# Optimization experiments

Hardware: AMD Instinct MI355X
Metric: run time of the kernel (lower is better)

## Reference

```python
import jax, jax.numpy as jnp
import numpy as np

NUM_EMBEDDINGS = 1024
EMBEDDING_DIM = 512
COMMITMENT_COST = 0.25


def setup_inputs() -> dict:
    key = jax.random.key(0)
    k1, k2 = jax.random.split(key)
    z_e = jax.random.normal(k1, (32, EMBEDDING_DIM, 32, 32), dtype=jnp.float32)
    # nn.Embedding weight, initialized normal (EMA branch: decay > 0)
    embedding = jax.random.normal(k2, (NUM_EMBEDDINGS, EMBEDDING_DIM), dtype=jnp.float32)
    return {"z_e": z_e, "embedding": embedding}


def reference(z_e, embedding):
    # z_e: [B, D, H, W] -> [B, H, W, D]
    ze = jnp.transpose(z_e, (0, 2, 3, 1))
    B, H, W, D = ze.shape
    K = embedding.shape[0]
    flat = ze.reshape(-1, D)  # [N, D]

    distances = (
        jnp.sum(flat * flat, axis=1, keepdims=True)
        + jnp.sum(embedding * embedding, axis=1)
        - 2.0 * jnp.matmul(flat, embedding.T)
    )
    indices = jnp.argmin(distances, axis=1)  # [N]

    # one-hot encodings (returned, and used for perplexity) -- matmul with
    # codebook is equivalent to a gather, so use the gather for z_q
    encodings = jax.nn.one_hot(indices, K, dtype=flat.dtype)  # [N, K]
    z_q = embedding[indices].reshape(B, H, W, D)

    # EMA branch (decay > 0): loss is commitment loss only
    e_latent_loss = jnp.mean((jax.lax.stop_gradient(z_q) - ze) ** 2)
    loss = COMMITMENT_COST * e_latent_loss

    # straight-through estimator
    z_q_st = ze + jax.lax.stop_gradient(z_q - ze)

    avg_probs = jnp.mean(encodings, axis=0)  # [K]
    perplexity = jnp.exp(-jnp.sum(avg_probs * jnp.log(avg_probs + 1e-10)))

    z_q_out = jnp.transpose(z_q_st, (0, 3, 1, 2))  # back to [B, D, H, W]
    return z_q_out, loss, perplexity, encodings
```

## Files before the change

### kernel.cpp

```cpp
#include <hip/hip_runtime.h>
#include <stdint.h>

#define B_ 32
#define D_ 512
#define P_ 1024
#define N_ 32768
#define K_ 1024

#define GAP_THR 0.75f

typedef unsigned long long u64;
typedef __attribute__((ext_vector_type(8))) short short8;
typedef __attribute__((ext_vector_type(4))) float float4v;

__device__ __forceinline__ unsigned fkey(float f) {
    unsigned u = __float_as_uint(f);
    return (u & 0x80000000u) ? ~u : (u | 0x80000000u);
}
__device__ __forceinline__ float funkey(unsigned k) {
    unsigned u = (k & 0x80000000u) ? (k & 0x7fffffffu) : ~k;
    return __uint_as_float(u);
}
__device__ __forceinline__ unsigned short f2bf(float x) {
    unsigned u = __float_as_uint(x);
    unsigned r = (u + 0x7fffu + ((u >> 16) & 1u)) >> 16;
    return (unsigned short)r;
}
__device__ __forceinline__ float bf2f(unsigned short h) {
    return __uint_as_float(((unsigned)h) << 16);
}

#define GLOAD_LDS16(gsrc, ldst) \
    __builtin_amdgcn_global_load_lds((const __attribute__((address_space(1))) unsigned int*)(const void*)(gsrc), \
                                     (__attribute__((address_space(3))) unsigned int*)(void*)(ldst), 16, 0, 0)

__global__ __launch_bounds__(256) void k_prep(const float* __restrict__ z,
                                              unsigned short* __restrict__ Xhi,
                                              const float* __restrict__ emb,
                                              unsigned short* __restrict__ Ehi,
                                              float* __restrict__ ET,
                                              float* __restrict__ enorm,
                                              double* __restrict__ enormD,
                                              int* __restrict__ counts,
                                              int* __restrict__ flagCount) {
    __shared__ float Zl[128][67];
    int tid = threadIdx.x;

    if (blockIdx.x >= 256) {
        int base = (blockIdx.x - 256) * 8;
        if (tid < 8) counts[base + tid] = 0;
        if (blockIdx.x == 256 && tid == 0) *flagCount = 0;
        int wave = tid >> 6, lane = tid & 63;
        float* Es = &Zl[0][0];
        #pragma unroll
        for (int cc = 0; cc < 2; ++cc) {
            int ci = wave * 2 + cc;
            int c = base + ci;
            const float4* row = (const float4*)(emb + (size_t)c * D_);
            float4 a = row[lane * 2];
            float4 b2 = row[lane * 2 + 1];
            float xs[8] = {a.x, a.y, a.z, a.w, b2.x, b2.y, b2.z, b2.w};
            unsigned short h[8];
            double s = 0.0;
            #pragma unroll
            for (int j = 0; j < 8; ++j) {
                h[j] = f2bf(xs[j]);
                Es[ci * 513 + lane * 8 + j] = xs[j];
                double d = (double)xs[j];
                s += d * d;
            }
            uint4 w;
            w.x = (unsigned)h[0] | ((unsigned)h[1] << 16);
            w.y = (unsigned)h[2] | ((unsigned)h[3] << 16);
            w.z = (unsigned)h[4] | ((unsigned)h[5] << 16);
            w.w = (unsigned)h[6] | ((unsigned)h[7] << 16);
            *(uint4*)(Ehi + (size_t)c * D_ + lane * 8) = w;
            #pragma unroll
            for (int off = 32; off; off >>= 1) s += __shfl_down(s, off, 64);
            if (lane == 0) { enorm[c] = (float)s; enormD[c] = s; }
        }
        __syncthreads();
        #pragma unroll
        for (int g = 0; g < 2; ++g) {
            int d = g * 256 + tid;
            float v[8];
            #pragma unroll
            for (int cc = 0; cc < 8; ++cc) v[cc] = Es[cc * 513 + d];
            float4* dst = (float4*)(ET + (size_t)d * 1024 + base);
            dst[0] = make_float4(v[0], v[1], v[2], v[3]);
            dst[1] = make_float4(v[4], v[5], v[6], v[7]);
        }
        return;
    }

    int b = blockIdx.x >> 3, pt = blockIdx.x & 7;
    int p0 = pt * 128;
    int t0 = b * P_ + p0;
    const float* zb = z + ((size_t)b * D_) * P_ + p0;
    int c8 = tid & 7, pp = tid >> 3;

    for (int dc = 0; dc < 8; ++dc) {
        int d0 = dc * 64;
        __syncthreads();
        #pragma unroll
        for (int jj = 0; jj < 8; ++jj) {
            int flat = jj * 256 + tid;
            int d = flat >> 5, p4 = flat & 31;
            float4 v = *(const float4*)(zb + (size_t)(d0 + d) * P_ + p4 * 4);
            Zl[p4 * 4 + 0][d] = v.x;
            Zl[p4 * 4 + 1][d] = v.y;
            Zl[p4 * 4 + 2][d] = v.z;
            Zl[p4 * 4 + 3][d] = v.w;
        }
        __syncthreads();
        #pragma unroll
        for (int g = 0; g < 4; ++g) {
            int p = pp + g * 32;
            unsigned short hh[8];
            #pragma unroll
            for (int j = 0; j < 8; ++j) hh[j] = f2bf(Zl[p][c8 * 8 + j]);
            uint4 w;
            w.x = (unsigned)hh[0] | ((unsigned)hh[1] << 16);
            w.y = (unsigned)hh[2] | ((unsigned)hh[3] << 16);
            w.z = (unsigned)hh[4] | ((unsigned)hh[5] << 16);
            w.w = (unsigned)hh[6] | ((unsigned)hh[7] << 16);
            *(uint4*)(Xhi + (size_t)(t0 + p) * D_ + d0 + c8 * 8) = w;
        }
    }
}

__global__ __launch_bounds__(512, 2) void k_gemm(const unsigned short* __restrict__ Xhi,
                                                 const unsigned short* __restrict__ Ehi,
                                                 const float* __restrict__ enorm,
                                                 u64* __restrict__ part) {
    __shared__ __align__(16) char smem[131072];
    const int tid = threadIdx.x;
    const int wave = tid >> 6, lane = tid & 63;
    const int lr = lane & 15, lg = lane >> 4;
    const int wr = wave >> 2, wc = wave & 3;
    const int work = (blockIdx.x & 7) * 64 + (blockIdx.x >> 3);
    const int rb = work >> 2, cb = work & 3;
    const int t0 = rb * 256, c0 = cb * 256;

    float4v acc[8][4];
    #pragma unroll
    for (int i = 0; i < 8; ++i)
        #pragma unroll
        for (int j = 0; j < 4; ++j)
            acc[i][j] = (float4v){0.f, 0.f, 0.f, 0.f};

    auto stageHalf = [&](int h) {
        if (h >= 32) return;
        int T = h >> 2, j = h & 3;
        int khalf = j >> 1, isB = j & 1;
        const unsigned short* plane = isB ? Xhi : Ehi;
        int row0 = isB ? t0 : c0;
        int kseg = T * 64 + khalf * 32;
        char* region = smem + (T & 1) * 65536 + isB * 32768 + khalf * 16384;
        #pragma unroll
        for (int jj = 0; jj < 2; ++jj) {
            int o = jj * 8192 + wave * 1024 + lane * 16;
            int pair = o >> 7;
            int sl = ((o >> 4) & 7) ^ (pair & 7);
            int row = pair * 2 + (sl >> 2);
            int k8 = sl & 3;
            GLOAD_LDS16(plane + (size_t)(row0 + row) * D_ + kseg + k8 * 8,
                        region + jj * 8192 + wave * 1024);
        }
    };

    for (int h = 0; h < 6; ++h) stageHalf(h);

    for (int t = 0; t < 8; ++t) {
        const int buf = t & 1;
        const char* Ab = smem + buf * 65536;
        const char* Bb = smem + buf * 65536 + 32768;
        if (t < 7) { asm volatile("s_waitcnt vmcnt(4)" ::: "memory"); }
        else       { asm volatile("s_waitcnt vmcnt(0)" ::: "memory"); }
        __builtin_amdgcn_s_barrier();
        __builtin_amdgcn_sched_barrier(0);
        #pragma unroll
        for (int q = 0; q < 4; ++q) {
            const int ks = q >> 1, mq = q & 1;
            const char* Ar = Ab + ks * 16384;
            const char* Br = Bb + ks * 16384;
            short8 af[4], bf[4];
            #pragma unroll
            for (int i = 0; i < 4; ++i) {
                int arow = wr * 128 + (mq * 4 + i) * 16 + lr;
                int ap = arow >> 1;
                int as_ = (((arow & 1) << 2) | lg) ^ (ap & 7);
                af[i] = *(const short8*)(Ar + ap * 128 + as_ * 16);
            }
            #pragma unroll
            for (int i = 0; i < 4; ++i) {
                int brow = wc * 64 + i * 16 + lr;
                int bp = brow >> 1;
                int bs_ = (((brow & 1) << 2) | lg) ^ (bp & 7);
                bf[i] = *(const short8*)(Br + bp * 128 + bs_ * 16);
            }
            stageHalf(4 * t + q + 6);
            __builtin_amdgcn_sched_barrier(0);
            __builtin_amdgcn_s_barrier();
            asm volatile("s_waitcnt lgkmcnt(0)" ::: "memory");
            __builtin_amdgcn_sched_barrier(0);
            __builtin_amdgcn_s_setprio(1);
            #pragma unroll
            for (int i = 0; i < 4; ++i)
                #pragma unroll
                for (int j = 0; j < 4; ++j)
                    acc[mq * 4 + i][j] = __builtin_amdgcn_mfma_f32_16x16x32_bf16(af[i], bf[j], acc[mq * 4 + i][j], 0, 0, 0);
            __builtin_amdgcn_s_setprio(0);
            __builtin_amdgcn_s_barrier();
        }
    }

    float en[8][4];
    #pragma unroll
    for (int mi = 0; mi < 8; ++mi)
        #pragma unroll
        for (int rr = 0; rr < 4; ++rr)
            en[mi][rr] = enorm[c0 + wr * 128 + mi * 16 + lg * 4 + rr];

    #pragma unroll
    for (int ni = 0; ni < 4; ++ni) {
        float v1 = 3.4e38f, v2 = 3.4e38f;
        int c1 = 0;
        #pragma unroll
        for (int mi = 0; mi < 8; ++mi) {
            #pragma unroll
            for (int rr = 0; rr < 4; ++rr) {
                float dist = fmaf(-2.f, acc[mi][ni][rr], en[mi][rr]);
                int code = c0 + wr * 128 + mi * 16 + lg * 4 + rr;
                if (dist < v1) { v2 = v1; v1 = dist; c1 = code; }
                else v2 = fminf(v2, dist);
            }
        }
        #pragma unroll
        for (int mask = 16; mask <= 32; mask <<= 1) {
            float ov1 = __shfl_xor(v1, mask, 64);
            int   oc1 = __shfl_xor(c1, mask, 64);
            float ov2 = __shfl_xor(v2, mask, 64);
            bool take = (ov1 < v1) || (ov1 == v1 && oc1 < c1);
            float loser = take ? v1 : ov1;
            v2 = fminf(fminf(v2, ov2), loser);
            if (take) { v1 = ov1; c1 = oc1; }
        }
        if (lg == 0) {
            int t = t0 + wc * 64 + ni * 16 + lr;
            ulonglong2 pk;
            pk.x = ((u64)fkey(v1) << 32) | (unsigned)c1;
            pk.y = ((u64)fkey(v2) << 32);
            *(ulonglong2*)&part[((size_t)t * 8 + cb * 2 + wr) * 2] = pk;
        }
    }
}

__global__ __launch_bounds__(256) void k_merge(const u64* __restrict__ part,
                                               int* __restrict__ indices,
                                               int* __restrict__ flags,
                                               int* __restrict__ flagCount) {
    int t = blockIdx.x * 256 + threadIdx.x;
    ulonglong2 a0 = *(const ulonglong2*)&part[(size_t)t * 16];
    u64 m1 = a0.x;
    float m2v = funkey((unsigned)(a0.y >> 32));
    for (int s = 1; s < 8; ++s) {
        ulonglong2 a = *(const ulonglong2*)&part[((size_t)t * 8 + s) * 2];
        float ax = funkey((unsigned)(a.x >> 32));
        float ay = funkey((unsigned)(a.y >> 32));
        if (a.x < m1) { m2v = fminf(m2v, funkey((unsigned)(m1 >> 32))); m1 = a.x; }
        else m2v = fminf(m2v, ax);
        m2v = fminf(m2v, ay);
    }
    indices[t] = (int)(m1 & 0xffffffffu);
    float v1 = funkey((unsigned)(m1 >> 32));
    if (m2v - v1 < GAP_THR) {
        int pos = atomicAdd(flagCount, 1);
        if (pos < N_) flags[pos] = t;
    }
}

__global__ __launch_bounds__(256) void k_repair(const float* __restrict__ z,
                                                const float* __restrict__ ET,
                                                const double* __restrict__ enormD,
                                                const int* __restrict__ flags,
                                                const int* __restrict__ flagCount,
                                                int* __restrict__ indices) {
    __shared__ double zl[4][512];
    __shared__ double rv[256];
    __shared__ int rc[256];
    const int tid = threadIdx.x;
    int nf = *flagCount;
    if (nf > N_) nf = N_;
    int nb = (nf + 3) >> 2;
    for (int bi = blockIdx.x; bi < nb; bi += gridDim.x) {
        int base = bi * 4;
        int ntok = nf - base; if (ntok > 4) ntok = 4;
        __syncthreads();
        for (int i = tid; i < 2048; i += 256) {
            int g = i >> 9, d = i & 511;
            if (g < ntok) {
                int t = flags[base + g];
                zl[g][d] = (double)z[(size_t)(t >> 10) * (D_ * P_) + (size_t)d * P_ + (t & 1023)];
            } else {
                zl[g][d] = 0.0;
            }
        }
        __syncthreads();

        double acc[4][4];
        #pragma unroll
        for (int g = 0; g < 4; ++g)
            #pragma unroll
            for (int k = 0; k < 4; ++k) acc[g][k] = 0.0;

        #pragma unroll 4
        for (int d = 0; d < 512; ++d) {
            const float* ep = ET + (size_t)d * 1024 + tid;
            double e0 = (double)ep[0];
            double e1 = (double)ep[256];
            double e2 = (double)ep[512];
            double e3 = (double)ep[768];
            double z0 = zl[0][d], z1 = zl[1][d], z2 = zl[2][d], z3 = zl[3][d];
            acc[0][0] = fma(e0, z0, acc[0][0]);
            acc[0][1] = fma(e1, z0, acc[0][1]);
            acc[0][2] = fma(e2, z0, acc[0][2]);
            acc[0][3] = fma(e3, z0, acc[0][3]);
            acc[1][0] = fma(e0, z1, acc[1][0]);
            acc[1][1] = fma(e1, z1, acc[1][1]);
            acc[1][2] = fma(e2, z1, acc[1][2]);
            acc[1][3] = fma(e3, z1, acc[1][3]);
            acc[2][0] = fma(e0, z2, acc[2][0]);
            acc[2][1] = fma(e1, z2, acc[2][1]);
            acc[2][2] = fma(e2, z2, acc[2][2]);
            acc[2][3] = fma(e3, z2, acc[2][3]);
            acc[3][0] = fma(e0, z3, acc[3][0]);
            acc[3][1] = fma(e1, z3, acc[3][1]);
            acc[3][2] = fma(e2, z3, acc[3][2]);
            acc[3][3] = fma(e3, z3, acc[3][3]);
        }

        for (int g = 0; g < ntok; ++g) {
            double bv = 1e300;
            int bc = 0;
            #pragma unroll
            for (int k = 0; k < 4; ++k) {
                int c = k * 256 + tid;
                double dist = enormD[c] - 2.0 * acc[g][k];
                if (dist < bv) { bv = dist; bc = c; }
            }
            rv[tid] = bv; rc[tid] = bc;
            __syncthreads();
            for (int st = 128; st; st >>= 1) {
                if (tid < st) {
                    if (rv[tid + st] < rv[tid] ||
                        (rv[tid + st] == rv[tid] && rc[tid + st] < rc[tid])) {
                        rv[tid] = rv[tid + st]; rc[tid] = rc[tid + st];
                    }
                }
                __syncthreads();
            }
            if (tid == 0) indices[flags[base + g]] = rc[0];
            __syncthreads();
        }
    }
}

__global__ __launch_bounds__(256) void k_out(const int* __restrict__ indices,
                                             float* __restrict__ enc,
                                             int* __restrict__ counts,
                                             const float* __restrict__ z,
                                             const float* __restrict__ emb,
                                             float* __restrict__ zq,
                                             float* __restrict__ lossp) {
    int tid = threadIdx.x;
    if (blockIdx.x < 4096) {
        int r = blockIdx.x * 8 + (tid >> 5);
        int l = tid & 31;
        int idx = indices[r];
        if (l == 0) atomicAdd(&counts[idx], 1);
        float4* rowp = (float4*)(enc + (size_t)r * K_);
        #pragma unroll
        for (int i = 0; i < 8; ++i) {
            int c4 = i * 32 + l;
            int base = c4 * 4;
            float4 v;
            v.x = (idx == base) ? 1.f : 0.f;
            v.y = (idx == base + 1) ? 1.f : 0.f;
            v.z = (idx == base + 2) ? 1.f : 0.f;
            v.w = (idx == base + 3) ? 1.f : 0.f;
            rowp[c4] = v;
        }
        return;
    }
    int gid = (blockIdx.x - 4096) * 256 + tid;
    int p4 = gid & 255;
    int rest = gid >> 8;
    int d = rest & 511;
    int b = rest >> 9;
    int p = p4 * 4;
    size_t zoff = (size_t)b * (D_ * P_) + (size_t)d * P_ + p;
    float4 zv = *(const float4*)(z + zoff);
    int nbase = b * P_ + p;
    int i0 = indices[nbase + 0];
    int i1 = indices[nbase + 1];
    int i2 = indices[nbase + 2];
    int i3 = indices[nbase + 3];
    float e0 = emb[(size_t)i0 * D_ + d];
    float e1 = emb[(size_t)i1 * D_ + d];
    float e2 = emb[(size_t)i2 * D_ + d];
    float e3 = emb[(size_t)i3 * D_ + d];
    float d0 = e0 - zv.x;
    float d1 = e1 - zv.y;
    float d2 = e2 - zv.z;
    float d3 = e3 - zv.w;
    float4 o;
    o.x = zv.x + d0; o.y = zv.y + d1; o.z = zv.z + d2; o.w = zv.w + d3;
    *(float4*)(zq + zoff) = o;
    float s = d0 * d0 + d1 * d1 + d2 * d2 + d3 * d3;
    #pragma unroll
    for (int off = 32; off; off >>= 1) s += __shfl_down(s, off, 64);
    __shared__ float wsum[4];
    if ((tid & 63) == 0) wsum[tid >> 6] = s;
    __syncthreads();
    if (tid == 0) lossp[blockIdx.x - 4096] = wsum[0] + wsum[1] + wsum[2] + wsum[3];
}

__global__ __launch_bounds__(1024) void k_final(const float* __restrict__ lossp,
                                                const int* __restrict__ counts,
                                                float* __restrict__ out_loss,
                                                float* __restrict__ out_perp) {
    int tid = threadIdx.x;
    float s = 0.f;
    for (int i = tid; i < 16384; i += 1024) s += lossp[i];
    #pragma unroll
    for (int off = 32; off; off >>= 1) s += __shfl_down(s, off, 64);
    __shared__ float red[16];
    if ((tid & 63) == 0) red[tid >> 6] = s;

    float pr = (float)counts[tid] * (1.f / 32768.f);
    float term = pr * logf(pr + 1e-10f);
    #pragma unroll
    for (int off = 32; off; off >>= 1) term += __shfl_down(term, off, 64);
    __shared__ float red2[16];
    if ((tid & 63) == 0) red2[tid >> 6] = term;
    __syncthreads();
    if (tid == 0) {
        float tot = 0.f;
        for (int i = 0; i < 16; ++i) tot += red[i];
        *out_loss = 0.25f * (tot / 16777216.f);
        float t2 = 0.f;
        for (int i = 0; i < 16; ++i) t2 += red2[i];
        *out_perp = expf(-t2);
    }
}

extern "C" void kernel_launch(void* const* d_in, const int* in_sizes, int n_in,
                              void* d_out, int out_size, void* d_ws, size_t ws_size,
                              hipStream_t stream) {
    const float* z   = (const float*)d_in[0];
    const float* emb = (const float*)d_in[1];

    float* zq       = (float*)d_out;
    float* out_loss = zq + 16777216;
    float* out_perp = zq + 16777217;
    float* enc      = zq + 16777218;

    char* ws = (char*)d_ws;
    float* enorm   = (float*)ws;
    int* counts    = (int*)(ws + 4096);
    int* flagCount = (int*)(ws + 8192);
    double* enormD = (double*)(ws + 16384);
    int* flags     = (int*)(ws + 24576);
    int* indices   = (int*)(ws + 24576 + 131072);
    float* lossp   = (float*)(ws + 24576 + 262144);

    char* sb = (char*)d_out + 67108880;
    unsigned short* Xhi  = (unsigned short*)(sb);
    unsigned short* EhiP = (unsigned short*)(sb + 33554432);
    u64* part = (u64*)(sb + 34603008);
    float* ET = (float*)(sb + 38797312);

    k_prep<<<384, 256, 0, stream>>>(z, Xhi, emb, EhiP, ET, enorm, enormD, counts, flagCount);
    k_gemm<<<512, 512, 0, stream>>>(Xhi, EhiP, enorm, part);
    k_merge<<<128, 256, 0, stream>>>(part, indices, flags, flagCount);
    k_repair<<<512, 256, 0, stream>>>(z, ET, enormD, flags, flagCount, indices);
    k_out<<<20480, 256, 0, stream>>>(indices, enc, counts, z, emb, zq, lossp);
    k_final<<<1, 1024, 0, stream>>>(lossp, counts, out_loss, out_perp);
}
```

Measured before the change: 233.4 us.

## Stage gathered codebook rows in LDS to coalesce z_q output gather

Each z_q block now covers 128 spatial positions of one batch and loops over eight 64-wide channel chunks. It loads the selected codebook rows contiguously with float4 reads into padded shared memory, then reads them transposed while streaming z and writing z_q. This replaces scattered per-element codebook loads (stride D across positions) with coalesced row reads. The cost is fewer blocks (256 instead of 16384), extra barriers and LDS traffic. The loss partial count and the final reduction are adjusted to match.

After: 210.2 us, median of 2. -10.0%, faster.

```diff
diff --git a/kernel.cpp b/kernel.cpp
--- a/kernel.cpp
+++ b/kernel.cpp
@@ -393,37 +393,56 @@
         }
         return;
     }
-    int gid = (blockIdx.x - 4096) * 256 + tid;
-    int p4 = gid & 255;
-    int rest = gid >> 8;
-    int d = rest & 511;
-    int b = rest >> 9;
-    int p = p4 * 4;
-    size_t zoff = (size_t)b * (D_ * P_) + (size_t)d * P_ + p;
-    float4 zv = *(const float4*)(z + zoff);
-    int nbase = b * P_ + p;
-    int i0 = indices[nbase + 0];
-    int i1 = indices[nbase + 1];
-    int i2 = indices[nbase + 2];
-    int i3 = indices[nbase + 3];
-    float e0 = emb[(size_t)i0 * D_ + d];
-    float e1 = emb[(size_t)i1 * D_ + d];
-    float e2 = emb[(size_t)i2 * D_ + d];
-    float e3 = emb[(size_t)i3 * D_ + d];
-    float d0 = e0 - zv.x;
-    float d1 = e1 - zv.y;
-    float d2 = e2 - zv.z;
-    float d3 = e3 - zv.w;
-    float4 o;
-    o.x = zv.x + d0; o.y = zv.y + d1; o.z = zv.z + d2; o.w = zv.w + d3;
-    *(float4*)(zq + zoff) = o;
-    float s = d0 * d0 + d1 * d1 + d2 * d2 + d3 * d3;
+
+    __shared__ int sIdx[128];
+    __shared__ float El[128 * 65];
+    int gb = blockIdx.x - 4096;
+    int b = gb >> 3, pt = gb & 7;
+    int p0 = pt * 128;
+    if (tid < 128) sIdx[tid] = indices[b * P_ + p0 + tid];
+    __syncthreads();
+
+    float lsum = 0.f;
+    for (int dc = 0; dc < 8; ++dc) {
+        int d0 = dc * 64;
+        #pragma unroll
+        for (int pass = 0; pass < 4; ++pass) {
+            int p = pass * 32 + (tid >> 3);
+            int l8 = tid & 7;
+            const float* er = emb + (size_t)sIdx[p] * D_ + d0 + l8 * 8;
+            float4 e0 = *(const float4*)er;
+            float4 e1 = *(const float4*)(er + 4);
+            int base = p * 65 + l8 * 8;
+            El[base + 0] = e0.x; El[base + 1] = e0.y;
+            El[base + 2] = e0.z; El[base + 3] = e0.w;
+            El[base + 4] = e1.x; El[base + 5] = e1.y;
+            El[base + 6] = e1.z; El[base + 7] = e1.w;
+        }
+        __syncthreads();
+        #pragma unroll
+        for (int it = 0; it < 8; ++it) {
+            int f = it * 256 + tid;
+            int d = f >> 5, p4 = f & 31;
+            size_t zoff = (size_t)b * (D_ * P_) + (size_t)(d0 + d) * P_ + p0 + p4 * 4;
+            float4 zv = *(const float4*)(z + zoff);
+            float e0 = El[(p4 * 4 + 0) * 65 + d];
+            float e1 = El[(p4 * 4 + 1) * 65 + d];
+            float e2 = El[(p4 * 4 + 2) * 65 + d];
+            float e3 = El[(p4 * 4 + 3) * 65 + d];
+            float q0 = e0 - zv.x, q1 = e1 - zv.y, q2 = e2 - zv.z, q3 = e3 - zv.w;
+            float4 o;
+            o.x = zv.x + q0; o.y = zv.y + q1; o.z = zv.z + q2; o.w = zv.w + q3;
+            *(float4*)(zq + zoff) = o;
+            lsum += q0 * q0 + q1 * q1 + q2 * q2 + q3 * q3;
+        }
+        __syncthreads();
+    }
     #pragma unroll
-    for (int off = 32; off; off >>= 1) s += __shfl_down(s, off, 64);
+    for (int off = 32; off; off >>= 1) lsum += __shfl_down(lsum, off, 64);
     __shared__ float wsum[4];
-    if ((tid & 63) == 0) wsum[tid >> 6] = s;
+    if ((tid & 63) == 0) wsum[tid >> 6] = lsum;
     __syncthreads();
-    if (tid == 0) lossp[blockIdx.x - 4096] = wsum[0] + wsum[1] + wsum[2] + wsum[3];
+    if (tid == 0) lossp[gb] = wsum[0] + wsum[1] + wsum[2] + wsum[3];
 }
 
 __global__ __launch_bounds__(1024) void k_final(const float* __restrict__ lossp,
@@ -431,8 +450,7 @@
                                                 float* __restrict__ out_loss,
                                                 float* __restrict__ out_perp) {
     int tid = threadIdx.x;
-    float s = 0.f;
-    for (int i = tid; i < 16384; i += 1024) s += lossp[i];
+    float s = (tid < 256) ? lossp[tid] : 0.f;
     #pragma unroll
     for (int off = 32; off; off >>= 1) s += __shfl_down(s, off, 64);
     __shared__ float red[16];
@@ -485,6 +503,6 @@
     k_gemm<<<512, 512, 0, stream>>>(Xhi, EhiP, enorm, part);
     k_merge<<<128, 256, 0, stream>>>(part, indices, flags, flagCount);
     k_repair<<<512, 256, 0, stream>>>(z, ET, enormD, flags, flagCount, indices);
-    k_out<<<20480, 256, 0, stream>>>(indices, enc, counts, z, emb, zq, lossp);
+    k_out<<<4352, 256, 0, stream>>>(indices, enc, counts, z, emb, zq, lossp);
     k_final<<<1, 1024, 0, stream>>>(lossp, counts, out_loss, out_perp);
 }
```
